# Performance work log

Hardware: AMD Instinct MI355X
Metric: run time of the kernel (lower is better)

The kernel has to match this reference:

```python
import jax, jax.numpy as jnp
import numpy as np

B, C, T = 32, 512, 2048
OUT_SEQ_LEN = 80
SIGMA2 = 10.0


def setup_inputs() -> dict:
    key = jax.random.key(0)
    k1, k2, k3, k4, k5, k6 = jax.random.split(key, 6)
    x = jax.random.normal(k1, (B, C, T), dtype=jnp.float32)
    # lengths in [T//2, T], with at least one equal to T (torch broadcast assumes max(len)==T)
    len_fea = jax.random.randint(k2, (B,), T // 2, T + 1)
    len_fea = len_fea.at[0].set(T)
    s1 = 1.0 / np.sqrt(C)
    conv1_w = jax.random.uniform(k3, (C, C), jnp.float32, -s1, s1)   # 1x1 conv == linear [out,in]
    conv1_b = jax.random.uniform(k4, (C,), jnp.float32, -s1, s1)
    conv2_w = jax.random.uniform(k5, (C,), jnp.float32, -s1, s1)     # out_channels=1, squeezed
    conv2_b = jax.random.uniform(k6, (), jnp.float32, -s1, s1)
    return {"x": x, "len_fea": len_fea, "conv1_w": conv1_w, "conv1_b": conv1_b,
            "conv2_w": conv2_w, "conv2_b": conv2_b}


def reference(x, len_fea, conv1_w, conv1_b, conv2_w, conv2_b):
    b_size, _, Tt = x.shape
    unaligned = x  # [B,C,T]
    h = jax.nn.relu(x)
    h = jnp.einsum('oc,bct->bot', conv1_w, h) + conv1_b[None, :, None]  # 1x1 conv
    h = jax.nn.relu(h)
    g = jnp.einsum('c,bct->bt', conv2_w, h) + conv2_b                   # 1x1 conv to 1 channel
    g = jax.nn.sigmoid(g)                                               # rec=True path
    gls_ends = jnp.cumsum(g, axis=1)            # [B,T]
    gls_centers = gls_ends - g * 0.5            # [B,T]
    aligned_lengths = gls_ends[jnp.arange(b_size), len_fea - 1]         # [B]
    out_pos = 0.5 + jnp.arange(OUT_SEQ_LEN, dtype=x.dtype)              # rec=True positions
    w = gls_centers[:, None, :] - out_pos[None, :, None]                # [B,L,T]
    w = -(w * w) / SIGMA2
    mask = (jnp.arange(Tt)[None, :] >= len_fea[:, None]).astype(x.dtype)  # [B,T]
    w = w - 1e9 * mask[:, None, :]
    w = jax.nn.softmax(w, axis=-1)
    aligned_features = jnp.einsum('blt,bct->blc', w, unaligned)         # [B,L,C]
    return aligned_features, aligned_lengths
```

## Files before the change

### kernel.cpp

```cpp
#include <hip/hip_runtime.h>
#include <hip/hip_bf16.h>

#define NB 32
#define NC 512
#define NT 2048
#define NL 80
static constexpr float kInvSigma2 = 0.1f;

typedef __attribute__((ext_vector_type(8))) __bf16 bf16x8;
typedef __attribute__((ext_vector_type(4))) float f32x4;

__device__ __forceinline__ void gld_lds16(const void* gp, void* lp) {
  __builtin_amdgcn_global_load_lds(
      (const __attribute__((address_space(1))) unsigned int*)gp,
      (__attribute__((address_space(3))) unsigned int*)lp, 16, 0, 0);
}

__global__ __launch_bounds__(256) void k_w1p(const float* __restrict__ w1,
                                             __hip_bfloat16* __restrict__ w1p) {
  const int q = blockIdx.x * 256 + threadIdx.x;
  const int c_lo = (q & 3) << 3;
  const int o_lo = (q >> 2) & 15;
  const int c5 = (q >> 6) & 15;
  const int o4 = q >> 10;
  const int o = (o4 << 4) + o_lo;
  const int c = (c5 << 5) + c_lo;
  const float4 p0 = *reinterpret_cast<const float4*>(&w1[o * NC + c]);
  const float4 p1 = *reinterpret_cast<const float4*>(&w1[o * NC + c + 4]);
  bf16x8 v;
  v[0] = (__bf16)p0.x; v[1] = (__bf16)p0.y;
  v[2] = (__bf16)p0.z; v[3] = (__bf16)p0.w;
  v[4] = (__bf16)p1.x; v[5] = (__bf16)p1.y;
  v[6] = (__bf16)p1.z; v[7] = (__bf16)p1.w;
  *reinterpret_cast<bf16x8*>(&w1p[(size_t)q * 8]) = v;
}

__global__ __launch_bounds__(256) void k_xT(const float* __restrict__ x,
                                            __hip_bfloat16* __restrict__ xT) {
  __shared__ __hip_bfloat16 ts[64][64];
  const int blk = blockIdx.x;
  const int b = blk >> 8;
  const int c0 = ((blk >> 5) & 7) << 6;
  const int t0 = (blk & 31) << 6;
  const int tid = threadIdx.x;

  const int cg = tid >> 4;
  const int tl = (tid & 15) << 2;
#pragma unroll
  for (int i = 0; i < 4; ++i) {
    const int c = (i << 4) + cg;
    const float4 v = *reinterpret_cast<const float4*>(
        &x[((size_t)b * NC + c0 + c) * NT + t0 + tl]);
    const __hip_bfloat16 u[4] = {
        __float2bfloat16(fmaxf(v.x, 0.f)), __float2bfloat16(fmaxf(v.y, 0.f)),
        __float2bfloat16(fmaxf(v.z, 0.f)), __float2bfloat16(fmaxf(v.w, 0.f))};
#pragma unroll
    for (int j = 0; j < 4; ++j) {
      const int t = tl + j;
      const int phys = ((((c >> 3) ^ (t & 7)) << 3) | (c & 7));
      ts[t][phys] = u[j];
    }
  }
  __syncthreads();

  const int tr = tid >> 3;
  const int gc = tid & 7;
#pragma unroll
  for (int j = 0; j < 2; ++j) {
    const int t = (j << 5) + tr;
    const int pg = gc ^ (t & 7);
    const bf16x8 vv = *reinterpret_cast<const bf16x8*>(&ts[t][pg << 3]);
    *reinterpret_cast<bf16x8*>(
        &xT[((size_t)b * NT + t0 + t) * NC + c0 + (gc << 3)]) = vv;
  }
}

__global__ __launch_bounds__(512, 4) void k_g_mfma(
    const __hip_bfloat16* __restrict__ xT, const __hip_bfloat16* __restrict__ w1p,
    const float* __restrict__ b1, const float* __restrict__ w2,
    const float* __restrict__ b2, float* __restrict__ g) {
  __shared__ __hip_bfloat16 bs[64 * 512];
  __shared__ float pws[8][64];
  const int blk = blockIdx.x;
  const int b = blk >> 5;
  const int t0 = (blk & 31) << 6;
  const int tid = threadIdx.x;
  const int w = tid >> 6;
  const int lane = tid & 63;
  const int ln = tid & 15;
  const int kg = lane >> 4;
  const int ob = w << 6;

  {
    const char* xrow0 = (const char*)(xT + ((size_t)(b * NT + t0) * NC));
    for (int r = w; r < 64; r += 8) {
      const int cb = ((lane << 4) ^ ((r & 7) << 4));
      gld_lds16(xrow0 + ((size_t)r << 10) + cb, (char*)bs + (r << 10));
    }
  }
  asm volatile("s_waitcnt vmcnt(0)" ::: "memory");
  __syncthreads();

  f32x4 acc[4][4];
#pragma unroll
  for (int ot = 0; ot < 4; ++ot)
#pragma unroll
    for (int nt = 0; nt < 4; ++nt) acc[ot][nt] = (f32x4){0.f, 0.f, 0.f, 0.f};

  int rowb[4], xm[4];
#pragma unroll
  for (int nt = 0; nt < 4; ++nt) {
    const int tr = (nt << 4) + ln;
    rowb[nt] = tr << 10;
    xm[nt] = (tr & 7) << 4;
  }
  const __hip_bfloat16* abase =
      w1p + ((size_t)w << 15) + (ln << 5) + (kg << 3);
  const char* bsb = (const char*)bs;

#pragma unroll 4
  for (int ks = 0; ks < 16; ++ks) {
    const int gb = (ks << 6) + (kg << 4);
    bf16x8 bfrag[4];
#pragma unroll
    for (int nt = 0; nt < 4; ++nt)
      bfrag[nt] = *reinterpret_cast<const bf16x8*>(
          bsb + rowb[nt] + (gb ^ xm[nt]));
#pragma unroll
    for (int ot = 0; ot < 4; ++ot) {
      const bf16x8 af = *reinterpret_cast<const bf16x8*>(
          abase + (ot << 13) + (ks << 9));
#pragma unroll
      for (int nt = 0; nt < 4; ++nt)
        acc[ot][nt] = __builtin_amdgcn_mfma_f32_16x16x32_bf16(
            af, bfrag[nt], acc[ot][nt], 0, 0, 0);
    }
  }

  float pl[4] = {0.f, 0.f, 0.f, 0.f};
#pragma unroll
  for (int ot = 0; ot < 4; ++ot) {
    const int o4 = ob + (ot << 4) + (kg << 2);
    const float4 b1v = *reinterpret_cast<const float4*>(&b1[o4]);
    const float4 w2v = *reinterpret_cast<const float4*>(&w2[o4]);
#pragma unroll
    for (int nt = 0; nt < 4; ++nt) {
      pl[nt] = fmaf(w2v.x, fmaxf(acc[ot][nt][0] + b1v.x, 0.f), pl[nt]);
      pl[nt] = fmaf(w2v.y, fmaxf(acc[ot][nt][1] + b1v.y, 0.f), pl[nt]);
      pl[nt] = fmaf(w2v.z, fmaxf(acc[ot][nt][2] + b1v.z, 0.f), pl[nt]);
      pl[nt] = fmaf(w2v.w, fmaxf(acc[ot][nt][3] + b1v.w, 0.f), pl[nt]);
    }
  }
#pragma unroll
  for (int nt = 0; nt < 4; ++nt) {
    pl[nt] += __shfl_xor(pl[nt], 16, 64);
    pl[nt] += __shfl_xor(pl[nt], 32, 64);
  }
  if (kg == 0) {
#pragma unroll
    for (int nt = 0; nt < 4; ++nt) pws[w][(nt << 4) + ln] = pl[nt];
  }
  __syncthreads();
  if (tid < 64) {
    float s = b2[0];
#pragma unroll
    for (int i = 0; i < 8; ++i) s += pws[i][tid];
    g[b * NT + t0 + tid] = 1.f / (1.f + __expf(-s));
  }
}

__global__ __launch_bounds__(256) void k_g_slow(const float* __restrict__ x,
                                                const float* __restrict__ w1,
                                                const float* __restrict__ b1,
                                                const float* __restrict__ w2,
                                                const float* __restrict__ b2,
                                                float* __restrict__ g) {
  __shared__ __hip_bfloat16 xs[NC][64];
  const int blk = blockIdx.x;
  const int b = blk >> 5;
  const int t0 = (blk & 31) << 6;
  const int tid = threadIdx.x;
  {
    const int tl = (tid & 15) << 2;
    const int c0 = tid >> 4;
    for (int c = c0; c < NC; c += 16) {
      const float4 v = *reinterpret_cast<const float4*>(
          &x[((size_t)b * NC + c) * NT + t0 + tl]);
      xs[c][tl + 0] = __float2bfloat16(fmaxf(v.x, 0.f));
      xs[c][tl + 1] = __float2bfloat16(fmaxf(v.y, 0.f));
      xs[c][tl + 2] = __float2bfloat16(fmaxf(v.z, 0.f));
      xs[c][tl + 3] = __float2bfloat16(fmaxf(v.w, 0.f));
    }
  }
  __syncthreads();
  const int og = tid >> 6;
  const int t = tid & 63;
  float gacc = 0.f;
  for (int pass = 0; pass < 16; ++pass) {
    const int o0 = (og << 7) + (pass << 3);
    float h[8];
#pragma unroll
    for (int j = 0; j < 8; ++j) h[j] = b1[o0 + j];
    const float* wrow = w1 + (size_t)o0 * NC;
#pragma unroll 4
    for (int c = 0; c < NC; ++c) {
      const float xv = __bfloat162float(xs[c][t]);
#pragma unroll
      for (int j = 0; j < 8; ++j) h[j] = fmaf(wrow[j * NC + c], xv, h[j]);
    }
    float p = 0.f;
#pragma unroll
    for (int j = 0; j < 8; ++j) p = fmaf(w2[o0 + j], fmaxf(h[j], 0.f), p);
    gacc += p;
  }
  __syncthreads();
  float* gr = reinterpret_cast<float*>(&xs[0][0]);
  gr[og * 64 + t] = gacc;
  __syncthreads();
  if (tid < 64) {
    const float s = gr[tid] + gr[64 + tid] + gr[128 + tid] + gr[192 + tid] + b2[0];
    g[b * NT + t0 + tid] = 1.f / (1.f + __expf(-s));
  }
}

__global__ __launch_bounds__(256) void k_scan(const float* __restrict__ g,
                                              const int* __restrict__ len_fea,
                                              float* __restrict__ centers,
                                              float* __restrict__ out_len) {
  const int b = blockIdx.x;
  const int tid = threadIdx.x;
  const float* gb = g + b * NT;
  float v[8];
  {
    const float4 p0 = *reinterpret_cast<const float4*>(&gb[tid * 8]);
    const float4 p1 = *reinterpret_cast<const float4*>(&gb[tid * 8 + 4]);
    v[0] = p0.x; v[1] = p0.y; v[2] = p0.z; v[3] = p0.w;
    v[4] = p1.x; v[5] = p1.y; v[6] = p1.z; v[7] = p1.w;
  }
  float s = 0.f;
#pragma unroll
  for (int j = 0; j < 8; ++j) s += v[j];
  float wscan = s;
  const int lane = tid & 63, wid = tid >> 6;
#pragma unroll
  for (int off = 1; off < 64; off <<= 1) {
    const float o = __shfl_up(wscan, (unsigned)off, 64);
    if (lane >= off) wscan += o;
  }
  __shared__ float wsum[4];
  if (lane == 63) wsum[wid] = wscan;
  __syncthreads();
  float base = 0.f;
#pragma unroll
  for (int i = 0; i < 4; ++i)
    if (i < wid) base += wsum[i];
  float run = base + wscan - s;
  const int li = len_fea[b] - 1;
#pragma unroll
  for (int j = 0; j < 8; ++j) {
    const int t = tid * 8 + j;
    run += v[j];
    centers[b * NT + t] = run - 0.5f * v[j];
    if (t == li) out_len[b] = run;
  }
}

__global__ __launch_bounds__(256) void k_wstats(
    const float* __restrict__ centers, const int* __restrict__ len_fea,
    __hip_bfloat16* __restrict__ wbf) {
  const int b = blockIdx.x / NL;
  const int l = blockIdx.x % NL;
  const int tid = threadIdx.x;
  const int len = len_fea[b];
  const float pos = 0.5f + (float)l;
  const float* cb = centers + b * NT;
  const int t0 = tid * 8;

  float cv[8];
  {
    const float4 p0 = *reinterpret_cast<const float4*>(&cb[t0]);
    const float4 p1 = *reinterpret_cast<const float4*>(&cb[t0 + 4]);
    cv[0] = p0.x; cv[1] = p0.y; cv[2] = p0.z; cv[3] = p0.w;
    cv[4] = p1.x; cv[5] = p1.y; cv[6] = p1.z; cv[7] = p1.w;
  }
  float lg[8];
  float m = -3.0e38f;
#pragma unroll
  for (int j = 0; j < 8; ++j) {
    if (t0 + j < len) {
      const float d = cv[j] - pos;
      lg[j] = -d * d * kInvSigma2;
      m = fmaxf(m, lg[j]);
    } else {
      lg[j] = -3.0e38f;
    }
  }
  const int lane = tid & 63, wid = tid >> 6;
#pragma unroll
  for (int off = 32; off > 0; off >>= 1) m = fmaxf(m, __shfl_xor(m, off, 64));
  __shared__ float redm[4];
  if (lane == 0) redm[wid] = m;
  __syncthreads();
  const float M = fmaxf(fmaxf(redm[0], redm[1]), fmaxf(redm[2], redm[3]));

  float e[8];
  float ssum = 0.f;
#pragma unroll
  for (int j = 0; j < 8; ++j) {
    e[j] = (t0 + j < len) ? __expf(lg[j] - M) : 0.f;
    ssum += e[j];
  }
#pragma unroll
  for (int off = 32; off > 0; off >>= 1) ssum += __shfl_xor(ssum, off, 64);
  __shared__ float reds[4];
  if (lane == 0) reds[wid] = ssum;
  __syncthreads();
  const float rinv = 1.f / (reds[0] + reds[1] + reds[2] + reds[3]);

  bf16x8 o;
#pragma unroll
  for (int j = 0; j < 8; ++j) o[j] = (__bf16)(e[j] * rinv);
  *reinterpret_cast<bf16x8*>(&wbf[((size_t)b * NL + l) * NT + t0]) = o;
}

__global__ __launch_bounds__(256) void k_out_mfma(
    const float* __restrict__ x, const __hip_bfloat16* __restrict__ wbf,
    float* __restrict__ out) {
  __shared__ float red[3][64][41];
  const int blk = blockIdx.x;
  const int b = blk >> 4;
  const int c0 = (blk & 15) << 5;
  const int tid = threadIdx.x;
  const int w = tid >> 6;
  const int lane = tid & 63;
  const int ln = tid & 15;
  const int kg = lane >> 4;
  const int tbase = w << 9;

  f32x4 acc[5][2];
#pragma unroll
  for (int lt = 0; lt < 5; ++lt)
#pragma unroll
    for (int nt = 0; nt < 2; ++nt) acc[lt][nt] = (f32x4){0.f, 0.f, 0.f, 0.f};

  const __hip_bfloat16* abase =
      wbf + ((size_t)b * NL + ln) * NT + tbase + (kg << 3);
  const float* bbase = x + ((size_t)b * NC + c0 + ln) * NT + tbase + (kg << 3);

#pragma unroll 4
  for (int ks = 0; ks < 16; ++ks) {
    const int ck = ks << 5;
    bf16x8 bfrag[2];
#pragma unroll
    for (int nt = 0; nt < 2; ++nt) {
      const float4 p0 =
          *reinterpret_cast<const float4*>(bbase + nt * 16 * NT + ck);
      const float4 p1 =
          *reinterpret_cast<const float4*>(bbase + nt * 16 * NT + ck + 4);
      bf16x8 v;
      v[0] = (__bf16)p0.x; v[1] = (__bf16)p0.y;
      v[2] = (__bf16)p0.z; v[3] = (__bf16)p0.w;
      v[4] = (__bf16)p1.x; v[5] = (__bf16)p1.y;
      v[6] = (__bf16)p1.z; v[7] = (__bf16)p1.w;
      bfrag[nt] = v;
    }
#pragma unroll
    for (int lt = 0; lt < 5; ++lt) {
      const bf16x8 af =
          *reinterpret_cast<const bf16x8*>(abase + lt * 16 * NT + ck);
      acc[lt][0] = __builtin_amdgcn_mfma_f32_16x16x32_bf16(af, bfrag[0],
                                                           acc[lt][0], 0, 0, 0);
      acc[lt][1] = __builtin_amdgcn_mfma_f32_16x16x32_bf16(af, bfrag[1],
                                                           acc[lt][1], 0, 0, 0);
    }
  }

  if (w > 0) {
#pragma unroll
    for (int lt = 0; lt < 5; ++lt)
#pragma unroll
      for (int nt = 0; nt < 2; ++nt)
#pragma unroll
        for (int j = 0; j < 4; ++j)
          red[w - 1][lane][lt * 8 + nt * 4 + j] = acc[lt][nt][j];
  }
  __syncthreads();
  if (w == 0) {
#pragma unroll
    for (int lt = 0; lt < 5; ++lt)
#pragma unroll
      for (int nt = 0; nt < 2; ++nt)
#pragma unroll
        for (int j = 0; j < 4; ++j) {
          float s = acc[lt][nt][j];
#pragma unroll
          for (int i = 0; i < 3; ++i) s += red[i][lane][lt * 8 + nt * 4 + j];
          const int l = lt * 16 + (kg << 2) + j;
          out[((size_t)b * NL + l) * NC + c0 + nt * 16 + ln] = s;
        }
  }
}

__global__ __launch_bounds__(256) void k_stats(const float* __restrict__ centers,
                                               const int* __restrict__ len_fea,
                                               float* __restrict__ rmax,
                                               float* __restrict__ rinv) {
  const int b = blockIdx.x / NL;
  const int l = blockIdx.x % NL;
  const int tid = threadIdx.x;
  const int len = len_fea[b];
  const float pos = 0.5f + (float)l;
  const float* cb = centers + b * NT;
  float lg[8];
  float m = -3.0e38f;
  const int t0 = tid * 8;
#pragma unroll
  for (int j = 0; j < 8; ++j) {
    const int t = t0 + j;
    if (t < len) {
      const float d = cb[t] - pos;
      lg[j] = -d * d * kInvSigma2;
      m = fmaxf(m, lg[j]);
    } else {
      lg[j] = -3.0e38f;
    }
  }
  const int lane = tid & 63, wid = tid >> 6;
#pragma unroll
  for (int off = 32; off > 0; off >>= 1) m = fmaxf(m, __shfl_xor(m, off, 64));
  __shared__ float redm[4];
  if (lane == 0) redm[wid] = m;
  __syncthreads();
  const float M = fmaxf(fmaxf(redm[0], redm[1]), fmaxf(redm[2], redm[3]));
  float ssum = 0.f;
#pragma unroll
  for (int j = 0; j < 8; ++j) {
    if (t0 + j < len) ssum += __expf(lg[j] - M);
  }
#pragma unroll
  for (int off = 32; off > 0; off >>= 1) ssum += __shfl_xor(ssum, off, 64);
  __shared__ float reds[4];
  if (lane == 0) reds[wid] = ssum;
  __syncthreads();
  if (tid == 0) {
    const float S = reds[0] + reds[1] + reds[2] + reds[3];
    rmax[blockIdx.x] = M;
    rinv[blockIdx.x] = 1.f / S;
  }
}

__global__ __launch_bounds__(128) void k_out(const float* __restrict__ x,
                                             const int* __restrict__ len_fea,
                                             const float* __restrict__ centers,
                                             const float* __restrict__ rmax,
                                             const float* __restrict__ rinv,
                                             float* __restrict__ out) {
  __shared__ float xsh[128][65];
  __shared__ float wsh[20][64];
  const int blk = blockIdx.x;
  const int b = blk >> 4;
  const int l0 = ((blk >> 2) & 3) * 20;
  const int c0 = (blk & 3) * 128;
  const int tid = threadIdx.x;
  const int len = len_fea[b];
  float acc[20];
#pragma unroll
  for (int l = 0; l < 20; ++l) acc[l] = 0.f;

  for (int t0 = 0; t0 < NT; t0 += 64) {
    __syncthreads();
    {
      const int tl = (tid & 15) << 2;
      const int r0 = tid >> 4;
      for (int r = r0; r < 128; r += 8) {
        const float4 v = *reinterpret_cast<const float4*>(
            &x[((size_t)b * NC + c0 + r) * NT + t0 + tl]);
        float* p = &xsh[r][tl];
        p[0] = v.x; p[1] = v.y; p[2] = v.z; p[3] = v.w;
      }
    }
#pragma unroll
    for (int k = 0; k < 10; ++k) {
      const int idx = k * 128 + tid;
      const int l = idx >> 6;
      const int tt = idx & 63;
      float wv = 0.f;
      if (t0 + tt < len) {
        const float d = centers[b * NT + t0 + tt] - (0.5f + (float)(l0 + l));
        wv = __expf(-d * d * kInvSigma2 - rmax[b * NL + l0 + l]) *
             rinv[b * NL + l0 + l];
      }
      wsh[l][tt] = wv;
    }
    __syncthreads();
#pragma unroll 4
    for (int tt = 0; tt < 64; ++tt) {
      const float xv = xsh[tid][tt];
#pragma unroll
      for (int l = 0; l < 20; ++l) acc[l] = fmaf(wsh[l][tt], xv, acc[l]);
    }
  }
#pragma unroll
  for (int l = 0; l < 20; ++l)
    out[((size_t)b * NL + l0 + l) * NC + c0 + tid] = acc[l];
}

extern "C" void kernel_launch(void* const* d_in, const int* in_sizes, int n_in,
                              void* d_out, int out_size, void* d_ws, size_t ws_size,
                              hipStream_t stream) {
  const float* x = (const float*)d_in[0];
  const int* len_fea = (const int*)d_in[1];
  const float* w1 = (const float*)d_in[2];
  const float* b1 = (const float*)d_in[3];
  const float* w2 = (const float*)d_in[4];
  const float* b2 = (const float*)d_in[5];

  float* out = (float*)d_out;
  float* out_len = out + (size_t)NB * NL * NC;

  float* ws = (float*)d_ws;
  float* g = ws;
  float* centers = ws + NB * NT;
  float* rmax = ws + 2 * NB * NT;
  float* rinv = rmax + NB * NL;
  __hip_bfloat16* w1p = (__hip_bfloat16*)(rinv + NB * NL);
  __hip_bfloat16* xT = w1p + (size_t)NC * NC;
  __hip_bfloat16* wbf = xT + (size_t)NB * NT * NC;

  const size_t need_mid = (size_t)(2 * NB * NT + 2 * NB * NL) * 4 +
                          ((size_t)NC * NC + (size_t)NB * NT * NC) * 2;
  const size_t need_full = need_mid + (size_t)NB * NL * NT * 2;

  if (ws_size >= need_full) {
    k_w1p<<<(NC * NC) / 2048, 256, 0, stream>>>(w1, w1p);
    k_xT<<<NB * 256, 256, 0, stream>>>(x, xT);
    k_g_mfma<<<NB * 32, 512, 0, stream>>>(xT, w1p, b1, w2, b2, g);
    k_scan<<<NB, 256, 0, stream>>>(g, len_fea, centers, out_len);
    k_wstats<<<NB * NL, 256, 0, stream>>>(centers, len_fea, wbf);
    k_out_mfma<<<NB * 16, 256, 0, stream>>>(x, wbf, out);
  } else if (ws_size >= need_mid) {
    k_w1p<<<(NC * NC) / 2048, 256, 0, stream>>>(w1, w1p);
    k_xT<<<NB * 256, 256, 0, stream>>>(x, xT);
    k_g_mfma<<<NB * 32, 512, 0, stream>>>(xT, w1p, b1, w2, b2, g);
    k_scan<<<NB, 256, 0, stream>>>(g, len_fea, centers, out_len);
    k_stats<<<NB * NL, 256, 0, stream>>>(centers, len_fea, rmax, rinv);
    k_out<<<NB * 16, 128, 0, stream>>>(x, len_fea, centers, rmax, rinv, out);
  } else {
    k_g_slow<<<NB * 32, 256, 0, stream>>>(x, w1, b1, w2, b2, g);
    k_scan<<<NB, 256, 0, stream>>>(g, len_fea, centers, out_len);
    k_stats<<<NB * NL, 256, 0, stream>>>(centers, len_fea, rmax, rinv);
    k_out<<<NB * 16, 128, 0, stream>>>(x, len_fea, centers, rmax, rinv, out);
  }
}
```

Baseline: 126.7 us.

## Fuse ReLU/bf16 transpose of x into the conv1 MFMA kernel's LDS staging

Removes the separate k_xT kernel that wrote a bf16 transposed copy of x to global memory. The conv1 MFMA kernel now reads fp32 x directly, applies ReLU, converts pairs of channels to packed bf16 and writes them into the swizzled LDS tile itself. This drops a full write and re-read of a 64 MB-scale intermediate and one kernel launch. In exchange, the g kernel's load phase reads twice the bytes (fp32) and no longer uses async global-to-LDS loads, so it relies on ordinary register loads and scattered 4-byte LDS stores.

```diff
diff --git a/kernel.cpp b/kernel.cpp
--- a/kernel.cpp
+++ b/kernel.cpp
@@ -9,12 +9,6 @@
 
 typedef __attribute__((ext_vector_type(8))) __bf16 bf16x8;
 typedef __attribute__((ext_vector_type(4))) float f32x4;
-
-__device__ __forceinline__ void gld_lds16(const void* gp, void* lp) {
-  __builtin_amdgcn_global_load_lds(
-      (const __attribute__((address_space(1))) unsigned int*)gp,
-      (__attribute__((address_space(3))) unsigned int*)lp, 16, 0, 0);
-}
 
 __global__ __launch_bounds__(256) void k_w1p(const float* __restrict__ w1,
                                              __hip_bfloat16* __restrict__ w1p) {
@@ -35,48 +29,8 @@
   *reinterpret_cast<bf16x8*>(&w1p[(size_t)q * 8]) = v;
 }
 
-__global__ __launch_bounds__(256) void k_xT(const float* __restrict__ x,
-                                            __hip_bfloat16* __restrict__ xT) {
-  __shared__ __hip_bfloat16 ts[64][64];
-  const int blk = blockIdx.x;
-  const int b = blk >> 8;
-  const int c0 = ((blk >> 5) & 7) << 6;
-  const int t0 = (blk & 31) << 6;
-  const int tid = threadIdx.x;
-
-  const int cg = tid >> 4;
-  const int tl = (tid & 15) << 2;
-#pragma unroll
-  for (int i = 0; i < 4; ++i) {
-    const int c = (i << 4) + cg;
-    const float4 v = *reinterpret_cast<const float4*>(
-        &x[((size_t)b * NC + c0 + c) * NT + t0 + tl]);
-    const __hip_bfloat16 u[4] = {
-        __float2bfloat16(fmaxf(v.x, 0.f)), __float2bfloat16(fmaxf(v.y, 0.f)),
-        __float2bfloat16(fmaxf(v.z, 0.f)), __float2bfloat16(fmaxf(v.w, 0.f))};
-#pragma unroll
-    for (int j = 0; j < 4; ++j) {
-      const int t = tl + j;
-      const int phys = ((((c >> 3) ^ (t & 7)) << 3) | (c & 7));
-      ts[t][phys] = u[j];
-    }
-  }
-  __syncthreads();
-
-  const int tr = tid >> 3;
-  const int gc = tid & 7;
-#pragma unroll
-  for (int j = 0; j < 2; ++j) {
-    const int t = (j << 5) + tr;
-    const int pg = gc ^ (t & 7);
-    const bf16x8 vv = *reinterpret_cast<const bf16x8*>(&ts[t][pg << 3]);
-    *reinterpret_cast<bf16x8*>(
-        &xT[((size_t)b * NT + t0 + t) * NC + c0 + (gc << 3)]) = vv;
-  }
-}
-
 __global__ __launch_bounds__(512, 4) void k_g_mfma(
-    const __hip_bfloat16* __restrict__ xT, const __hip_bfloat16* __restrict__ w1p,
+    const float* __restrict__ x, const __hip_bfloat16* __restrict__ w1p,
     const float* __restrict__ b1, const float* __restrict__ w2,
     const float* __restrict__ b2, float* __restrict__ g) {
   __shared__ __hip_bfloat16 bs[64 * 512];
@@ -92,13 +46,32 @@
   const int ob = w << 6;
 
   {
-    const char* xrow0 = (const char*)(xT + ((size_t)(b * NT + t0) * NC));
-    for (int r = w; r < 64; r += 8) {
-      const int cb = ((lane << 4) ^ ((r & 7) << 4));
-      gld_lds16(xrow0 + ((size_t)r << 10) + cb, (char*)bs + (r << 10));
-    }
-  }
-  asm volatile("s_waitcnt vmcnt(0)" ::: "memory");
+    const int tl = (tid & 15) << 2;
+    const int cp = (tid >> 4) << 1;
+    const float* xb = x + (size_t)b * NC * NT + t0;
+#pragma unroll
+    for (int i = 0; i < 8; ++i) {
+      const int c = (i << 6) + cp;
+      const float4 va =
+          *reinterpret_cast<const float4*>(&xb[(size_t)c * NT + tl]);
+      const float4 vb =
+          *reinterpret_cast<const float4*>(&xb[(size_t)(c + 1) * NT + tl]);
+      const float fa[4] = {va.x, va.y, va.z, va.w};
+      const float fb[4] = {vb.x, vb.y, vb.z, vb.w};
+#pragma unroll
+      for (int j = 0; j < 4; ++j) {
+        const int t = tl + j;
+        const __hip_bfloat16 lo = __float2bfloat16(fmaxf(fa[j], 0.f));
+        const __hip_bfloat16 hi = __float2bfloat16(fmaxf(fb[j], 0.f));
+        const unsigned pk =
+            ((unsigned)*reinterpret_cast<const unsigned short*>(&hi) << 16) |
+            *reinterpret_cast<const unsigned short*>(&lo);
+        *reinterpret_cast<unsigned*>(
+            (char*)bs + (t << 10) +
+            ((((c >> 3) ^ (t & 7)) << 4) | ((c & 7) << 1))) = pk;
+      }
+    }
+  }
   __syncthreads();
 
   f32x4 acc[4][4];
@@ -524,24 +497,21 @@
   float* rmax = ws + 2 * NB * NT;
   float* rinv = rmax + NB * NL;
   __hip_bfloat16* w1p = (__hip_bfloat16*)(rinv + NB * NL);
-  __hip_bfloat16* xT = w1p + (size_t)NC * NC;
-  __hip_bfloat16* wbf = xT + (size_t)NB * NT * NC;
+  __hip_bfloat16* wbf = w1p + (size_t)NC * NC;
 
   const size_t need_mid = (size_t)(2 * NB * NT + 2 * NB * NL) * 4 +
-                          ((size_t)NC * NC + (size_t)NB * NT * NC) * 2;
+                          (size_t)NC * NC * 2;
   const size_t need_full = need_mid + (size_t)NB * NL * NT * 2;
 
   if (ws_size >= need_full) {
     k_w1p<<<(NC * NC) / 2048, 256, 0, stream>>>(w1, w1p);
-    k_xT<<<NB * 256, 256, 0, stream>>>(x, xT);
-    k_g_mfma<<<NB * 32, 512, 0, stream>>>(xT, w1p, b1, w2, b2, g);
+    k_g_mfma<<<NB * 32, 512, 0, stream>>>(x, w1p, b1, w2, b2, g);
     k_scan<<<NB, 256, 0, stream>>>(g, len_fea, centers, out_len);
     k_wstats<<<NB * NL, 256, 0, stream>>>(centers, len_fea, wbf);
     k_out_mfma<<<NB * 16, 256, 0, stream>>>(x, wbf, out);
   } else if (ws_size >= need_mid) {
     k_w1p<<<(NC * NC) / 2048, 256, 0, stream>>>(w1, w1p);
-    k_xT<<<NB * 256, 256, 0, stream>>>(x, xT);
-    k_g_mfma<<<NB * 32, 512, 0, stream>>>(xT, w1p, b1, w2, b2, g);
+    k_g_mfma<<<NB * 32, 512, 0, stream>>>(x, w1p, b1, w2, b2, g);
     k_scan<<<NB, 256, 0, stream>>>(g, len_fea, centers, out_len);
     k_stats<<<NB * NL, 256, 0, stream>>>(centers, len_fea, rmax, rinv);
     k_out<<<NB * 16, 128, 0, stream>>>(x, len_fea, centers, rmax, rinv, out);
```

Measured after the change: 104.6 us. 1.21x faster.
